# Optimization experiments

Hardware: AMD Instinct MI355X
Metric: run time of the kernel (lower is better)

Reference implementation:

```python
import jax, jax.numpy as jnp
import numpy as np

N, D, F_NUM = 262144, 128, 64
TEMPERATURE = 0.5
EPS = 1e-8  # torch F.cosine_similarity eps


def setup_inputs() -> dict:
    key = jax.random.key(0)
    k1, k2 = jax.random.split(key)
    embeddings = jax.random.normal(k1, (N, D), dtype=jnp.float32)
    families = jax.random.randint(k2, (N,), 0, F_NUM, dtype=jnp.int32)
    return {"embeddings": embeddings, "families": families}


def reference(embeddings, families):
    T = TEMPERATURE
    n = embeddings.shape[0]
    # Per-family prototype means (segment mean). All F_NUM families are
    # present w.h.p.; guard counts with max(.,1) to avoid div-by-zero.
    ones = jnp.ones((n,), dtype=embeddings.dtype)
    counts = jax.ops.segment_sum(ones, families, num_segments=F_NUM)
    sums = jax.ops.segment_sum(embeddings, families, num_segments=F_NUM)
    protos = sums / jnp.maximum(counts, 1.0)[:, None]  # [F, D]

    # Cosine similarity matrix [N, F], matching torch eps semantics:
    # x.y / max(||x|| * ||y||, eps)
    dots = embeddings @ protos.T                              # [N, F]
    e_norm = jnp.linalg.norm(embeddings, axis=1)              # [N]
    p_norm = jnp.linalg.norm(protos, axis=1)                  # [F]
    sim = dots / jnp.maximum(e_norm[:, None] * p_norm[None, :], EPS)

    pos = jnp.take_along_axis(sim, families[:, None].astype(jnp.int32), axis=1)[:, 0]  # [N]
    # Source quirk: logits already divided by T, then divided by T again
    # inside logsumexp -> effective sim / T^2. The concatenated logits
    # contain pos + all other prototypes = all F prototypes exactly once.
    lse = jax.nn.logsumexp(sim / (T * T), axis=1)             # [N]
    per_sample = -pos / T + lse                               # [N]
    loss = jnp.sum(per_sample) / n
    return loss[None]  # torch returns shape (1,)
```

## Files before the change

### kernel.cpp

```cpp
#include <hip/hip_runtime.h>
#include <math.h>


#define D_DIM 128
#define F_NUM 64

typedef __attribute__((ext_vector_type(8))) short short8;
typedef __attribute__((ext_vector_type(4))) float f32x4;

static __device__ __forceinline__ unsigned short f2bf(float x) {
  union { float f; unsigned u; } v; v.f = x;
  unsigned r = v.u + 0x7FFFu + ((v.u >> 16) & 1u);
  return (unsigned short)(r >> 16);
}

__global__ __launch_bounds__(1024) void pass_a(
    const float* __restrict__ emb, const int* __restrict__ fam,
    float* __restrict__ psum, int* __restrict__ pcnt, int N)
{
  __shared__ float acc[16 * 64 * 32];
  __shared__ int lcnt[4 * F_NUM];
  int t = threadIdx.x;
  float4* acc4 = (float4*)acc;
  #pragma unroll
  for (int k = 0; k < 8; ++k) acc4[t + k * 1024] = make_float4(0.f,0.f,0.f,0.f);
  if (t < 4 * F_NUM) lcnt[t] = 0;
  __syncthreads();

  int w = t >> 6, l = t & 63;
  int s = w & 3, rep = w >> 2;
  int h = l >> 5, d = l & 31;
  int col = s * 32 + d;
  float* my = &acc[w * 2048];
  int B0 = blockIdx.x * 1024;
  int W0 = __builtin_amdgcn_readfirstlane(B0 + rep * 256);

  #pragma unroll 1
  for (int i = 0; i < 128; ++i) {
    int f0 = fam[W0 + 2 * i];
    int f1 = fam[W0 + 2 * i + 1];
    int row = W0 + 2 * i + h;
    float v = emb[(size_t)row * D_DIM + col];
    if (f0 == f1) {
      float vo = __shfl_xor(v, 32);
      if (h == 0) {
        my[f0 * 32 + d] += v + vo;
        if (s == 0 && d == 0) lcnt[rep * F_NUM + f0] += 2;
      }
    } else {
      int f = h ? f1 : f0;
      my[f * 32 + d] += v;
      if (s == 0 && d == 0) lcnt[rep * F_NUM + f] += 1;
    }
  }
  __syncthreads();

  float4* out4 = (float4*)(psum + (size_t)blockIdx.x * (F_NUM * D_DIM));
  #pragma unroll
  for (int k = 0; k < 2; ++k) {
    int idx4 = t + k * 1024;
    int f = idx4 >> 5, c4 = idx4 & 31;
    int sl = c4 >> 3, dd = (c4 & 7) << 2;
    float4 r = make_float4(0.f,0.f,0.f,0.f);
    #pragma unroll
    for (int rp = 0; rp < 4; ++rp) {
      float4 a = *(const float4*)&acc[(rp * 4 + sl) * 2048 + f * 32 + dd];
      r.x += a.x; r.y += a.y; r.z += a.z; r.w += a.w;
    }
    out4[idx4] = r;
  }
  if (t < F_NUM)
    pcnt[blockIdx.x * F_NUM + t] =
        lcnt[t] + lcnt[F_NUM + t] + lcnt[2 * F_NUM + t] + lcnt[3 * F_NUM + t];
}

__global__ __launch_bounds__(256) void pass_b(
    const float* __restrict__ psum, const int* __restrict__ pcnt,
    unsigned short* __restrict__ protoB, float* __restrict__ pinv)
{
  __shared__ float red[256];
  __shared__ float scnt;
  int f = blockIdx.x, t = threadIdx.x;
  int d = t & 127, h = t >> 7;

  red[t] = (float)pcnt[t * F_NUM + f];
  __syncthreads();
  for (int o = 128; o; o >>= 1) { if (t < o) red[t] += red[t + o]; __syncthreads(); }
  if (t == 0) scnt = fmaxf(red[0], 1.0f);
  __syncthreads();

  float s = 0.f;
  #pragma unroll 4
  for (int i = 0; i < 128; ++i)
    s += psum[(size_t)(h + 2 * i) * (F_NUM * D_DIM) + f * D_DIM + d];
  red[t] = s;
  __syncthreads();
  float proto = 0.f;
  if (t < 128) proto = (red[t] + red[t + 128]) / scnt;
  __syncthreads();

  red[t] = (t < 128) ? proto * proto : 0.f;
  __syncthreads();
  for (int o = 128; o; o >>= 1) { if (t < o) red[t] += red[t + o]; __syncthreads(); }
  if (t == 0) pinv[f] = rsqrtf(fmaxf(red[0], 1e-24f));

  if (t < 128) protoB[f * D_DIM + t] = f2bf(proto);
}

__global__ __launch_bounds__(256) void pass_c(
    const float* __restrict__ emb, const int* __restrict__ fam,
    const unsigned short* __restrict__ protoB, const float* __restrict__ pinv,
    float* __restrict__ bsums)
{
  __shared__ __align__(16) unsigned short sA[128 * 136];
  __shared__ __align__(16) unsigned short sB[F_NUM * 136];
  __shared__ float sInvE[128];
  __shared__ int   sFam[128];
  __shared__ float sWp[4];

  int t = threadIdx.x;
  int R0 = blockIdx.x * 128;
  const float4* src = (const float4*)emb;

  #pragma unroll
  for (int it = 0; it < 16; ++it) {
    int idx = it * 256 + t;
    int row = idx >> 5, c4 = idx & 31;
    float4 v = src[(size_t)(R0 + row) * 32 + c4];
    float nq = v.x * v.x + v.y * v.y + v.z * v.z + v.w * v.w;
    nq += __shfl_xor(nq, 1);  nq += __shfl_xor(nq, 2);  nq += __shfl_xor(nq, 4);
    nq += __shfl_xor(nq, 8);  nq += __shfl_xor(nq, 16);
    if ((t & 31) == 0) sInvE[row] = rsqrtf(nq);
    ushort4 u;
    u.x = f2bf(v.x); u.y = f2bf(v.y); u.z = f2bf(v.z); u.w = f2bf(v.w);
    *(ushort4*)&sA[row * 136 + (c4 << 2)] = u;
  }
  const ushort4* pb = (const ushort4*)protoB;
  #pragma unroll
  for (int it = 0; it < 8; ++it) {
    int idx = it * 256 + t;
    int f = idx >> 5, c4 = idx & 31;
    *(ushort4*)&sB[f * 136 + (c4 << 2)] = pb[idx];
  }
  if (t < 128) sFam[t] = fam[R0 + t];
  __syncthreads();

  int w = t >> 6, lane = t & 63, m16 = lane & 15, q = lane >> 4;
  float pv[4];
  #pragma unroll
  for (int ft = 0; ft < 4; ++ft) pv[ft] = pinv[ft * 16 + m16];

  f32x4 acc[2][4] = {};
  const unsigned short* aB0 = &sA[(w * 32 + m16) * 136 + q * 8];
  const unsigned short* aB1 = aB0 + 16 * 136;
  const unsigned short* bB  = &sB[m16 * 136 + q * 8];

  #pragma unroll
  for (int ks = 0; ks < 4; ++ks) {
    int ko = ks * 32;
    short8 a0 = *(const short8*)(aB0 + ko);
    short8 a1 = *(const short8*)(aB1 + ko);
    short8 b0 = *(const short8*)(bB + ko);
    short8 b1 = *(const short8*)(bB + 16 * 136 + ko);
    short8 b2 = *(const short8*)(bB + 32 * 136 + ko);
    short8 b3 = *(const short8*)(bB + 48 * 136 + ko);
    acc[0][0] = __builtin_amdgcn_mfma_f32_16x16x32_bf16(a0, b0, acc[0][0], 0, 0, 0);
    acc[0][1] = __builtin_amdgcn_mfma_f32_16x16x32_bf16(a0, b1, acc[0][1], 0, 0, 0);
    acc[0][2] = __builtin_amdgcn_mfma_f32_16x16x32_bf16(a0, b2, acc[0][2], 0, 0, 0);
    acc[0][3] = __builtin_amdgcn_mfma_f32_16x16x32_bf16(a0, b3, acc[0][3], 0, 0, 0);
    acc[1][0] = __builtin_amdgcn_mfma_f32_16x16x32_bf16(a1, b0, acc[1][0], 0, 0, 0);
    acc[1][1] = __builtin_amdgcn_mfma_f32_16x16x32_bf16(a1, b1, acc[1][1], 0, 0, 0);
    acc[1][2] = __builtin_amdgcn_mfma_f32_16x16x32_bf16(a1, b2, acc[1][2], 0, 0, 0);
    acc[1][3] = __builtin_amdgcn_mfma_f32_16x16x32_bf16(a1, b3, acc[1][3], 0, 0, 0);
  }

  float wp = 0.f;
  #pragma unroll
  for (int rt = 0; rt < 2; ++rt) {
    #pragma unroll
    for (int i = 0; i < 4; ++i) {
      int row = w * 32 + rt * 16 + q * 4 + i;
      float inv_e = sInvE[row];
      int fr = sFam[row], frh = fr >> 4, frl = fr & 15;
      float es = 0.f, ps = 0.f;
      #pragma unroll
      for (int ft = 0; ft < 4; ++ft) {
        float sim = acc[rt][ft][i] * inv_e * pv[ft];
        es += __expf(4.f * sim - 4.f);
        if (frl == m16 && frh == ft) ps = sim;
      }
      #pragma unroll
      for (int off = 1; off < 16; off <<= 1) {
        es += __shfl_xor(es, off);
        ps += __shfl_xor(ps, off);
      }
      if (m16 == 0) wp += 4.f + __logf(es) - 2.f * ps;
    }
  }
  wp += __shfl_xor(wp, 16);
  wp += __shfl_xor(wp, 32);
  if (lane == 0) sWp[w] = wp;
  __syncthreads();
  if (t == 0) bsums[blockIdx.x] = sWp[0] + sWp[1] + sWp[2] + sWp[3];
}

__global__ __launch_bounds__(256) void pass_d(
    const float* __restrict__ bs, float* __restrict__ out, int nb, float invN)
{
  __shared__ float red[256];
  int t = threadIdx.x;
  float s = 0.f;
  for (int i = t; i < nb; i += 256) s += bs[i];
  red[t] = s;
  __syncthreads();
  for (int o = 128; o; o >>= 1) { if (t < o) red[t] += red[t + o]; __syncthreads(); }
  if (t == 0) out[0] = red[0] * invN;
}

extern "C" void kernel_launch(void* const* d_in, const int* in_sizes, int n_in,
                              void* d_out, int out_size, void* d_ws, size_t ws_size,
                              hipStream_t stream) {
  const float* emb = (const float*)d_in[0];
  const int* fam = (const int*)d_in[1];
  int N = in_sizes[0] / D_DIM;
  int blocksA = N / 1024;
  int blocksC = N / 128;

  float* ws = (float*)d_ws;
  float* psum = ws;
  size_t off = (size_t)blocksA * (F_NUM * D_DIM);
  int* pcnt = (int*)(ws + off);              off += (size_t)blocksA * F_NUM;
  unsigned short* protoB = (unsigned short*)(ws + off); off += (F_NUM * D_DIM) / 2;
  float* pinv = ws + off;                    off += F_NUM;
  float* bsums = ws + off;

  pass_a<<<blocksA, 1024, 0, stream>>>(emb, fam, psum, pcnt, N);
  pass_b<<<F_NUM, 256, 0, stream>>>(psum, pcnt, protoB, pinv);
  pass_c<<<blocksC, 256, 0, stream>>>(emb, fam, protoB, pinv, bsums);
  pass_d<<<1, 256, 0, stream>>>(bsums, (float*)d_out, blocksC, 1.0f / (float)N);
}
```

Measured before the change: 291.8 us.

## Restructure segment-sum pass, widen prototype reduction, fold final reduction into atomics

The segment-sum kernel now runs 512 threads per block. Each wave covers 64 columns, and rows are processed in batches of 16 with the loads issued together, replacing the per-row-pair shuffle/branch loop. The prototype kernel uses 1024 threads with shallower reductions. The final reduce kernel is removed: each pass_c block atomically adds its scaled partial sum into the zeroed output. This trades fewer launches and better memory-level parallelism for more LDS per block and nondeterministic float summation order.

```diff
diff --git a/kernel.cpp b/kernel.cpp
--- a/kernel.cpp
+++ b/kernel.cpp
@@ -14,57 +14,55 @@
   return (unsigned short)(r >> 16);
 }
 
-__global__ __launch_bounds__(1024) void pass_a(
+__global__ __launch_bounds__(512) void pass_a(
     const float* __restrict__ emb, const int* __restrict__ fam,
-    float* __restrict__ psum, int* __restrict__ pcnt, int N)
+    float* __restrict__ psum, int* __restrict__ pcnt)
 {
-  __shared__ float acc[16 * 64 * 32];
+  __shared__ float acc[8 * 4096];
   __shared__ int lcnt[4 * F_NUM];
   int t = threadIdx.x;
-  float4* acc4 = (float4*)acc;
-  #pragma unroll
-  for (int k = 0; k < 8; ++k) acc4[t + k * 1024] = make_float4(0.f,0.f,0.f,0.f);
+  float4 z = make_float4(0.f, 0.f, 0.f, 0.f);
+  float4* a4 = (float4*)acc;
+  #pragma unroll
+  for (int k = 0; k < 16; ++k) a4[t + k * 512] = z;
   if (t < 4 * F_NUM) lcnt[t] = 0;
   __syncthreads();
 
   int w = t >> 6, l = t & 63;
-  int s = w & 3, rep = w >> 2;
-  int h = l >> 5, d = l & 31;
-  int col = s * 32 + d;
-  float* my = &acc[w * 2048];
-  int B0 = blockIdx.x * 1024;
-  int W0 = __builtin_amdgcn_readfirstlane(B0 + rep * 256);
+  int s = w & 1, rep = w >> 1;
+  float* my = acc + w * 4096;
+  int base = __builtin_amdgcn_readfirstlane(blockIdx.x * 1024 + rep * 256);
+  const float* ecol = emb + (size_t)base * D_DIM + s * 64 + l;
 
   #pragma unroll 1
-  for (int i = 0; i < 128; ++i) {
-    int f0 = fam[W0 + 2 * i];
-    int f1 = fam[W0 + 2 * i + 1];
-    int row = W0 + 2 * i + h;
-    float v = emb[(size_t)row * D_DIM + col];
-    if (f0 == f1) {
-      float vo = __shfl_xor(v, 32);
-      if (h == 0) {
-        my[f0 * 32 + d] += v + vo;
-        if (s == 0 && d == 0) lcnt[rep * F_NUM + f0] += 2;
-      }
-    } else {
-      int f = h ? f1 : f0;
-      my[f * 32 + d] += v;
-      if (s == 0 && d == 0) lcnt[rep * F_NUM + f] += 1;
+  for (int b = 0; b < 16; ++b) {
+    float v[16]; int f[16];
+    #pragma unroll
+    for (int j = 0; j < 16; ++j) {
+      int r = b * 16 + j;
+      v[j] = ecol[(size_t)r * D_DIM];
+      f[j] = fam[base + r];
+    }
+    #pragma unroll
+    for (int j = 0; j < 16; ++j)
+      my[f[j] * 64 + l] += v[j];
+    if (s == 0 && l == 0) {
+      #pragma unroll
+      for (int j = 0; j < 16; ++j) lcnt[rep * F_NUM + f[j]] += 1;
     }
   }
   __syncthreads();
 
   float4* out4 = (float4*)(psum + (size_t)blockIdx.x * (F_NUM * D_DIM));
   #pragma unroll
-  for (int k = 0; k < 2; ++k) {
-    int idx4 = t + k * 1024;
+  for (int k = 0; k < 4; ++k) {
+    int idx4 = t + k * 512;
     int f = idx4 >> 5, c4 = idx4 & 31;
-    int sl = c4 >> 3, dd = (c4 & 7) << 2;
-    float4 r = make_float4(0.f,0.f,0.f,0.f);
+    int ss = c4 >> 4, ll4 = (c4 & 15) << 2;
+    float4 r = z;
     #pragma unroll
     for (int rp = 0; rp < 4; ++rp) {
-      float4 a = *(const float4*)&acc[(rp * 4 + sl) * 2048 + f * 32 + dd];
+      float4 a = *(const float4*)&acc[(rp * 2 + ss) * 4096 + f * 64 + ll4];
       r.x += a.x; r.y += a.y; r.z += a.z; r.w += a.w;
     }
     out4[idx4] = r;
@@ -74,43 +72,58 @@
         lcnt[t] + lcnt[F_NUM + t] + lcnt[2 * F_NUM + t] + lcnt[3 * F_NUM + t];
 }
 
-__global__ __launch_bounds__(256) void pass_b(
+__global__ __launch_bounds__(1024) void pass_b(
     const float* __restrict__ psum, const int* __restrict__ pcnt,
     unsigned short* __restrict__ protoB, float* __restrict__ pinv)
 {
-  __shared__ float red[256];
+  __shared__ float red[1024];
+  __shared__ float rc[256];
+  __shared__ float prot[128];
   __shared__ float scnt;
   int f = blockIdx.x, t = threadIdx.x;
   int d = t & 127, h = t >> 7;
 
-  red[t] = (float)pcnt[t * F_NUM + f];
-  __syncthreads();
-  for (int o = 128; o; o >>= 1) { if (t < o) red[t] += red[t + o]; __syncthreads(); }
-  if (t == 0) scnt = fmaxf(red[0], 1.0f);
-  __syncthreads();
-
+  if (t < 256) rc[t] = (float)pcnt[t * F_NUM + f];
   float s = 0.f;
-  #pragma unroll 4
-  for (int i = 0; i < 128; ++i)
-    s += psum[(size_t)(h + 2 * i) * (F_NUM * D_DIM) + f * D_DIM + d];
+  #pragma unroll 8
+  for (int i = 0; i < 32; ++i)
+    s += psum[(size_t)(h + 8 * i) * (F_NUM * D_DIM) + f * D_DIM + d];
   red[t] = s;
   __syncthreads();
+  if (t < 128) {
+    float p = 0.f;
+    #pragma unroll
+    for (int hh = 0; hh < 8; ++hh) p += red[hh * 128 + d];
+    prot[d] = p;
+  }
+  if (t < 64) rc[t] += rc[t + 64] + rc[t + 128] + rc[t + 192];
+  __syncthreads();
+  if (t < 16) rc[t] += rc[t + 16] + rc[t + 32] + rc[t + 48];
+  __syncthreads();
+  if (t < 4) rc[t] += rc[t + 4] + rc[t + 8] + rc[t + 12];
+  __syncthreads();
+  if (t == 0) scnt = fmaxf(rc[0] + rc[1] + rc[2] + rc[3], 1.0f);
+  __syncthreads();
   float proto = 0.f;
-  if (t < 128) proto = (red[t] + red[t + 128]) / scnt;
-  __syncthreads();
-
-  red[t] = (t < 128) ? proto * proto : 0.f;
-  __syncthreads();
-  for (int o = 128; o; o >>= 1) { if (t < o) red[t] += red[t + o]; __syncthreads(); }
-  if (t == 0) pinv[f] = rsqrtf(fmaxf(red[0], 1e-24f));
-
+  if (t < 128) {
+    proto = prot[d] / scnt;
+    red[d] = proto * proto;
+  }
+  __syncthreads();
+  if (t < 32) red[t] += red[t + 32] + red[t + 64] + red[t + 96];
+  __syncthreads();
+  if (t < 8) red[t] += red[t + 8] + red[t + 16] + red[t + 24];
+  __syncthreads();
+  if (t < 2) red[t] += red[t + 2] + red[t + 4] + red[t + 6];
+  __syncthreads();
+  if (t == 0) pinv[f] = rsqrtf(fmaxf(red[0] + red[1], 1e-24f));
   if (t < 128) protoB[f * D_DIM + t] = f2bf(proto);
 }
 
 __global__ __launch_bounds__(256) void pass_c(
     const float* __restrict__ emb, const int* __restrict__ fam,
     const unsigned short* __restrict__ protoB, const float* __restrict__ pinv,
-    float* __restrict__ bsums)
+    float* __restrict__ out, float invN)
 {
   __shared__ __align__(16) unsigned short sA[128 * 136];
   __shared__ __align__(16) unsigned short sB[F_NUM * 136];
@@ -201,20 +214,8 @@
   wp += __shfl_xor(wp, 32);
   if (lane == 0) sWp[w] = wp;
   __syncthreads();
-  if (t == 0) bsums[blockIdx.x] = sWp[0] + sWp[1] + sWp[2] + sWp[3];
-}
-
-__global__ __launch_bounds__(256) void pass_d(
-    const float* __restrict__ bs, float* __restrict__ out, int nb, float invN)
-{
-  __shared__ float red[256];
-  int t = threadIdx.x;
-  float s = 0.f;
-  for (int i = t; i < nb; i += 256) s += bs[i];
-  red[t] = s;
-  __syncthreads();
-  for (int o = 128; o; o >>= 1) { if (t < o) red[t] += red[t + o]; __syncthreads(); }
-  if (t == 0) out[0] = red[0] * invN;
+  if (t == 0)
+    unsafeAtomicAdd(out, (sWp[0] + sWp[1] + sWp[2] + sWp[3]) * invN);
 }
 
 extern "C" void kernel_launch(void* const* d_in, const int* in_sizes, int n_in,
@@ -231,11 +232,11 @@
   size_t off = (size_t)blocksA * (F_NUM * D_DIM);
   int* pcnt = (int*)(ws + off);              off += (size_t)blocksA * F_NUM;
   unsigned short* protoB = (unsigned short*)(ws + off); off += (F_NUM * D_DIM) / 2;
-  float* pinv = ws + off;                    off += F_NUM;
-  float* bsums = ws + off;
-
-  pass_a<<<blocksA, 1024, 0, stream>>>(emb, fam, psum, pcnt, N);
-  pass_b<<<F_NUM, 256, 0, stream>>>(psum, pcnt, protoB, pinv);
-  pass_c<<<blocksC, 256, 0, stream>>>(emb, fam, protoB, pinv, bsums);
-  pass_d<<<1, 256, 0, stream>>>(bsums, (float*)d_out, blocksC, 1.0f / (float)N);
-}
+  float* pinv = ws + off;
+
+  hipMemsetAsync(d_out, 0, sizeof(float), stream);
+  pass_a<<<blocksA, 512, 0, stream>>>(emb, fam, psum, pcnt);
+  pass_b<<<F_NUM, 1024, 0, stream>>>(psum, pcnt, protoB, pinv);
+  pass_c<<<blocksC, 256, 0, stream>>>(emb, fam, protoB, pinv,
+                                      (float*)d_out, 1.0f / (float)N);
+}
```

Measured after the change: 252.1 us. 1.16x faster.
